# Kernel optimization log

Hardware: AMD Instinct MI355X
Metric: run time of the kernel (lower is better)

## Reference

```python
import jax, jax.numpy as jnp
import numpy as np

B, S, D = 2, 2048, 1024
H = 16
HD = D // H  # head_dim = 64


def setup_inputs() -> dict:
    key = jax.random.key(0)
    ks = jax.random.split(key, 6)
    scale = 0.02
    x = jax.random.normal(ks[0], (B, S, D), dtype=jnp.float32)
    Wq = jax.random.normal(ks[1], (D, D), dtype=jnp.float32) * scale
    Wk = jax.random.normal(ks[2], (D, D), dtype=jnp.float32) * scale
    Wv = jax.random.normal(ks[3], (D, D), dtype=jnp.float32) * scale
    Wo = jax.random.normal(ks[4], (D, D), dtype=jnp.float32) * scale
    bo = jax.random.normal(ks[5], (D,), dtype=jnp.float32) * scale
    return {"x": x, "Wq": Wq, "Wk": Wk, "Wv": Wv, "Wo": Wo, "bo": bo}


def reference(x, Wq, Wk, Wv, Wo, bo):
    b, s, d = x.shape
    # QKV projections (no bias, qkv_bias=False)
    Q = (x @ Wq).reshape(b, s, H, HD)
    K = (x @ Wk).reshape(b, s, H, HD)
    V = (x @ Wv).reshape(b, s, H, HD)
    # [b, h, q, k] attention scores
    scores = jnp.einsum('bqhd,bkhd->bhqk', Q, K)
    # causal mask: positions k > q masked to -inf (applied before scaling, as in source;
    # -inf / sqrt(hd) is still -inf so this matches)
    causal = jnp.triu(jnp.ones((s, s), dtype=bool), k=1)
    scores = jnp.where(causal, -jnp.inf, scores)
    att = jax.nn.softmax(scores / jnp.sqrt(jnp.float32(HD)), axis=-1)
    # dropout p=0.0 -> identity
    ctx = jnp.einsum('bhqk,bkhd->bqhd', att, V).reshape(b, s, d)
    return ctx @ Wo + bo
```

## Files before the change

kernel.cpp:

```cpp
#include <hip/hip_runtime.h>

typedef __bf16 bf16;
typedef __attribute__((ext_vector_type(8))) __bf16 bf16x8;
typedef __attribute__((ext_vector_type(4))) __bf16 bf16x4;
typedef __attribute__((ext_vector_type(4))) float floatx4;

#define MFMA16(a, b, c) __builtin_amdgcn_mfma_f32_16x16x32_bf16((a), (b), (c), 0, 0, 0)

static constexpr int BB = 2, SS = 2048, DD = 1024, HH = 16;
static constexpr int MM = BB * SS;
static constexpr int N_QKV = 3 * DD;

__device__ __forceinline__ float exp2c(float x) {
#if __has_builtin(__builtin_amdgcn_exp2f)
    return __builtin_amdgcn_exp2f(x);
#else
    return exp2f(x);
#endif
}

__device__ __forceinline__ void async16(const void* g, void* l) {
    __builtin_amdgcn_global_load_lds(
        (const __attribute__((address_space(1))) unsigned int*)g,
        (__attribute__((address_space(3))) unsigned int*)l, 16, 0, 0);
}

__global__ __launch_bounds__(256) void prep_kernel(const float* __restrict__ x,
                                                   bf16* __restrict__ xb,
                                                   const float* __restrict__ w0,
                                                   const float* __restrict__ w1,
                                                   const float* __restrict__ w2,
                                                   const float* __restrict__ w3,
                                                   bf16* __restrict__ outT) {
    const int blk = blockIdx.x, tid = threadIdx.x;
    if (blk < 4096) {
        int i = blk * 1024 + tid * 4;
        float4 v = *(const float4*)(x + i);
        bf16x4 o;
        o[0] = (bf16)v.x; o[1] = (bf16)v.y; o[2] = (bf16)v.z; o[3] = (bf16)v.w;
        *(bf16x4*)(xb + i) = o;
    } else {
        __shared__ float tile[32][33];
        const int wblk = blk - 4096;
        const int z = wblk >> 10, rem = wblk & 1023;
        const int by = rem >> 5, bx = rem & 31;
        const int tx = tid & 31, ty = tid >> 5;
        const float* src = (z == 0) ? w0 : (z == 1) ? w1 : (z == 2) ? w2 : w3;
        bf16* dst = outT + (size_t)z * DD * DD;
        int xc = bx * 32 + tx;
        int y0 = by * 32;
        for (int i = ty; i < 32; i += 8)
            tile[i][tx] = src[(size_t)(y0 + i) * DD + xc];
        __syncthreads();
        int xo = y0 + tx;
        int yo0 = bx * 32;
        for (int i = ty; i < 32; i += 8)
            dst[(size_t)(yo0 + i) * DD + xo] = (bf16)tile[tx][i];
    }
}

template <int BM, int BN, bool OUT_BF16, bool FUSE_VT>
__global__ __launch_bounds__(256) void gemm_kernel(const bf16* __restrict__ A,
                                                   const bf16* __restrict__ Bt,
                                                   void* __restrict__ C,
                                                   bf16* __restrict__ Vt_g,
                                                   const float* __restrict__ bias,
                                                   int K, int ldc) {
    constexpr int MT = BM / 32, NT = BN / 32;
    __shared__ bf16 As[BM * 64];
    __shared__ bf16 Bs[BN * 64];
    const int tid = threadIdx.x, wave = tid >> 6, lane = tid & 63;
    const int quad = lane >> 4, l16 = lane & 15;
    const int wm = wave >> 1, wn = wave & 1;
    const int m0 = blockIdx.y * BM, n0 = blockIdx.x * BN;
    const int l8r = lane >> 3, l8c = lane & 7;
    const int gch = ((l8c ^ l8r) * 8);

    floatx4 acc[MT][NT] = {};

    for (int k0 = 0; k0 < K; k0 += 64) {
        __syncthreads();
#pragma unroll
        for (int c = 0; c < BM / 32; ++c) {
            int r = wave * (BM / 4) + c * 8;
            async16(A + (size_t)(m0 + r + l8r) * K + k0 + gch, &As[r * 64]);
        }
#pragma unroll
        for (int c = 0; c < BN / 32; ++c) {
            int r = wave * (BN / 4) + c * 8;
            async16(Bt + (size_t)(n0 + r + l8r) * K + k0 + gch, &Bs[r * 64]);
        }
        __syncthreads();
#pragma unroll
        for (int cc = 0; cc < 2; ++cc) {
            bf16x8 af[MT], bv[NT];
#pragma unroll
            for (int i = 0; i < MT; ++i) {
                int row = wm * (BM / 2) + i * 16 + l16;
                af[i] = *(const bf16x8*)&As[row * 64 + ((cc * 4 + quad) ^ (row & 7)) * 8];
            }
#pragma unroll
            for (int j = 0; j < NT; ++j) {
                int row = wn * (BN / 2) + j * 16 + l16;
                bv[j] = *(const bf16x8*)&Bs[row * 64 + ((cc * 4 + quad) ^ (row & 7)) * 8];
            }
#pragma unroll
            for (int i = 0; i < MT; ++i)
#pragma unroll
                for (int j = 0; j < NT; ++j)
                    acc[i][j] = MFMA16(af[i], bv[j], acc[i][j]);
        }
    }

    if (FUSE_VT && n0 >= 2048) {
#pragma unroll
        for (int i = 0; i < MT; ++i)
#pragma unroll
            for (int j = 0; j < NT; ++j) {
                int grow = m0 + wm * (BM / 2) + i * 16 + quad * 4;
                int gcol = n0 + wn * (BN / 2) + j * 16 + l16;
                int bb = grow >> 11, s = grow & (SS - 1);
                int vcol = gcol - 2048;
                int hh = vcol >> 6, hd = vcol & 63;
                bf16x4 pk;
#pragma unroll
                for (int r = 0; r < 4; ++r) pk[r] = (bf16)acc[i][j][r];
                *(bf16x4*)&Vt_g[(((size_t)(bb * 16 + hh)) * 64 + hd) * SS + s] = pk;
            }
        return;
    }

#pragma unroll
    for (int i = 0; i < MT; ++i)
#pragma unroll
        for (int j = 0; j < NT; ++j)
#pragma unroll
            for (int r = 0; r < 4; ++r) {
                int row = m0 + wm * (BM / 2) + i * 16 + quad * 4 + r;
                int col = n0 + wn * (BN / 2) + j * 16 + l16;
                if (OUT_BF16)
                    ((bf16*)C)[(size_t)row * ldc + col] = (bf16)acc[i][j][r];
                else
                    ((float*)C)[(size_t)row * ldc + col] = acc[i][j][r] + bias[col];
            }
}

__global__ __launch_bounds__(256, 2) void attn_kernel(const bf16* __restrict__ QKV,
                                                      const bf16* __restrict__ Vt_g,
                                                      bf16* __restrict__ ctx) {
    __shared__ __align__(16) bf16 smem[24576];
    bf16* Ks = smem;
    bf16* Vt = smem + 8192;
    bf16* Ps = smem + 16384;
    bf16* Qs = Ps;

    const int tid = threadIdx.x, wave = tid >> 6, lane = tid & 63;
    const int quad = lane >> 4, l16 = lane & 15;
    const int gb = blockIdx.x;
    const int xcd = gb & 7, rr = gb >> 3;
    int bhl, t;
    if (rr < 32) { bhl = rr >> 4;              t = rr & 15; }
    else         { bhl = 2 + ((rr & 31) >> 4); t = 15 - (rr & 15); }
    const int bh = xcd * 4 + bhl;
    const int b = bh >> 4, h = bh & 15;
    const int q0 = t * 128;
    const size_t base = (size_t)(b * SS) * N_QKV;
    const bf16* Vg = Vt_g + (size_t)bh * 64 * SS;
    constexpr float C2 = 0.18033688011112042f;
    const int l8r = lane >> 3, l8c = lane & 7;
    const int gch = (l8c ^ l8r) * 8;
    const int swz = l16 & 7;
    const int nkt = 2 * t + 2;

    {
#pragma unroll
        for (int c = 0; c < 4; ++c) {
            int r0 = wave * 32 + c * 8;
            async16(QKV + base + (size_t)(q0 + r0 + l8r) * N_QKV + h * 64 + gch,
                    Qs + r0 * 64);
        }
#pragma unroll
        for (int c = 0; c < 2; ++c) {
            int r0 = wave * 16 + c * 8;
            async16(QKV + base + (size_t)(r0 + l8r) * N_QKV + DD + h * 64 + gch,
                    Ks + r0 * 64);
            async16(Vg + (size_t)(r0 + l8r) * SS + gch, Vt + r0 * 64);
        }
    }
    __syncthreads();

    bf16x8 qf[2][2];
#pragma unroll
    for (int gg = 0; gg < 2; ++gg)
#pragma unroll
        for (int cc = 0; cc < 2; ++cc) {
            int row = wave * 32 + gg * 16 + l16;
            qf[gg][cc] = *(const bf16x8*)&Qs[row * 64 + ((cc * 4 + quad) ^ swz) * 8];
        }

    bf16x8 onesf = {};
    if (l16 == 0) {
#pragma unroll
        for (int e = 0; e < 8; ++e) onesf[e] = (bf16)1.0f;
    }

    floatx4 accv[2][4] = {};
    floatx4 acc5[2] = {};
    const int qg0 = q0 + wave * 32 + l16;

    for (int kt = 0; kt < nkt; ++kt) {
        const int buf = kt & 1;
        if (kt + 1 < nkt) {
            const int k0n = (kt + 1) * 64;
            const int dst = (buf ^ 1) * 4096;
#pragma unroll
            for (int c = 0; c < 2; ++c) {
                int r0 = wave * 16 + c * 8;
                async16(QKV + base + (size_t)(k0n + r0 + l8r) * N_QKV + DD + h * 64 + gch,
                        Ks + dst + r0 * 64);
                async16(Vg + (size_t)(r0 + l8r) * SS + k0n + gch, Vt + dst + r0 * 64);
            }
        }
        const int k0 = kt * 64;

        floatx4 st[2][4];
#pragma unroll
        for (int j = 0; j < 4; ++j) { st[0][j] = (floatx4){}; st[1][j] = (floatx4){}; }
#pragma unroll
        for (int cc = 0; cc < 2; ++cc)
#pragma unroll
            for (int j = 0; j < 4; ++j) {
                bf16x8 kf = *(const bf16x8*)&Ks[buf * 4096 + (j * 16 + l16) * 64
                                                + ((cc * 4 + quad) ^ swz) * 8];
                st[0][j] = MFMA16(kf, qf[0][cc], st[0][j]);
                st[1][j] = MFMA16(kf, qf[1][cc], st[1][j]);
            }

        if (64 * kt + 63 > q0 + 32 * wave) {
#pragma unroll
            for (int gg = 0; gg < 2; ++gg) {
                const int qq = qg0 + gg * 16;
#pragma unroll
                for (int j = 0; j < 4; ++j) {
                    int kb = k0 + j * 16 + quad * 4;
#pragma unroll
                    for (int r = 0; r < 4; ++r)
                        if (kb + r > qq) st[gg][j][r] = -__builtin_inff();
                }
            }
        }

#pragma unroll
        for (int gg = 0; gg < 2; ++gg)
#pragma unroll
            for (int j = 0; j < 4; ++j) {
                bf16x4 pk4;
#pragma unroll
                for (int r = 0; r < 4; ++r)
                    pk4[r] = (bf16)exp2c(st[gg][j][r] * C2);
                *(bf16x4*)&Ps[wave * 2048 + gg * 1024 + l16 * 64
                              + ((2 * j + (quad >> 1)) ^ swz) * 8 + (quad & 1) * 4] = pk4;
            }

        bf16x8 pf[2][2];
#pragma unroll
        for (int gg = 0; gg < 2; ++gg)
#pragma unroll
            for (int cc = 0; cc < 2; ++cc)
                pf[gg][cc] = *(const bf16x8*)&Ps[wave * 2048 + gg * 1024 + l16 * 64
                                                 + ((cc * 4 + quad) ^ swz) * 8];
#pragma unroll
        for (int cc = 0; cc < 2; ++cc)
#pragma unroll
            for (int j = 0; j < 4; ++j) {
                bf16x8 vt = *(const bf16x8*)&Vt[buf * 4096 + (j * 16 + l16) * 64
                                                + ((cc * 4 + quad) ^ swz) * 8];
                accv[0][j] = MFMA16(pf[0][cc], vt, accv[0][j]);
                accv[1][j] = MFMA16(pf[1][cc], vt, accv[1][j]);
            }
        acc5[0] = MFMA16(pf[0][0], onesf, acc5[0]);
        acc5[0] = MFMA16(pf[0][1], onesf, acc5[0]);
        acc5[1] = MFMA16(pf[1][0], onesf, acc5[1]);
        acc5[1] = MFMA16(pf[1][1], onesf, acc5[1]);

        __syncthreads();
    }

#pragma unroll
    for (int gg = 0; gg < 2; ++gg) {
        float inv[4];
#pragma unroll
        for (int r = 0; r < 4; ++r)
            inv[r] = 1.0f / __shfl(acc5[gg][r], lane & 48, 64);
#pragma unroll
        for (int j = 0; j < 4; ++j)
#pragma unroll
            for (int r = 0; r < 4; ++r) {
                int row = b * SS + q0 + wave * 32 + gg * 16 + quad * 4 + r;
                int col = h * 64 + j * 16 + l16;
                ctx[(size_t)row * DD + col] = (bf16)(accv[gg][j][r] * inv[r]);
            }
    }
}

extern "C" void kernel_launch(void* const* d_in, const int* in_sizes, int n_in,
                              void* d_out, int out_size, void* d_ws, size_t ws_size,
                              hipStream_t stream) {
    const float* x  = (const float*)d_in[0];
    const float* Wq = (const float*)d_in[1];
    const float* Wk = (const float*)d_in[2];
    const float* Wv = (const float*)d_in[3];
    const float* Wo = (const float*)d_in[4];
    const float* bo = (const float*)d_in[5];
    float* out = (float*)d_out;

    char* ws = (char*)d_ws;
    bf16* xb   = (bf16*)ws;
    bf16* WT   = (bf16*)(ws + (size_t)(8  << 20));
    bf16* QKV  = (bf16*)(ws + (size_t)(16 << 20));
    bf16* ctxb = (bf16*)(ws + (size_t)(40 << 20));
    bf16* Vt_g = (bf16*)(ws + (size_t)(48 << 20));

    prep_kernel<<<dim3(8192), dim3(256), 0, stream>>>(x, xb, Wq, Wk, Wv, Wo, WT);
    gemm_kernel<128, 128, true, true><<<dim3(N_QKV / 128, MM / 128), dim3(256), 0, stream>>>(
        xb, WT, QKV, Vt_g, nullptr, DD, N_QKV);
    attn_kernel<<<dim3(512), dim3(256), 0, stream>>>(QKV, Vt_g, ctxb);
    gemm_kernel<128, 64, false, false><<<dim3(DD / 64, MM / 128), dim3(256), 0, stream>>>(
        ctxb, WT + (size_t)3 * DD * DD, out, nullptr, bo, DD, DD);
}
```

Baseline: 173.4 us.

## Shrink attention query tile to 64 rows and double the grid

The attention kernel now handles 64 query rows per block (16 per wave) instead of 128, so it launches 1024 blocks. The per-block LDS footprint shrinks and launch bounds ask for 4 blocks per CU, which should raise occupancy and give finer load balance across the causal triangle. The block-to-tile mapping is reworked with a zigzag pattern across 32 tiles, and masking now runs only on the diagonal tile. In exchange each K/V tile loaded into LDS is reused by half as many query rows, so K/V traffic per unit of work roughly doubles.

```diff
diff --git a/kernel.cpp b/kernel.cpp
--- a/kernel.cpp
+++ b/kernel.cpp
@@ -145,10 +145,10 @@
             }
 }
 
-__global__ __launch_bounds__(256, 2) void attn_kernel(const bf16* __restrict__ QKV,
+__global__ __launch_bounds__(256, 4) void attn_kernel(const bf16* __restrict__ QKV,
                                                       const bf16* __restrict__ Vt_g,
                                                       bf16* __restrict__ ctx) {
-    __shared__ __align__(16) bf16 smem[24576];
+    __shared__ __align__(16) bf16 smem[20480];
     bf16* Ks = smem;
     bf16* Vt = smem + 8192;
     bf16* Ps = smem + 16384;
@@ -158,30 +158,26 @@
     const int quad = lane >> 4, l16 = lane & 15;
     const int gb = blockIdx.x;
     const int xcd = gb & 7, rr = gb >> 3;
-    int bhl, t;
-    if (rr < 32) { bhl = rr >> 4;              t = rr & 15; }
-    else         { bhl = 2 + ((rr & 31) >> 4); t = 15 - (rr & 15); }
-    const int bh = xcd * 4 + bhl;
+    const int hi = rr >> 5, lo = rr & 31;
+    const int t = (hi == 0) ? lo : (hi == 1) ? (31 - lo)
+                : (hi == 2) ? (lo ^ 16) : (31 - (lo ^ 16));
+    const int bh = xcd * 4 + hi;
     const int b = bh >> 4, h = bh & 15;
-    const int q0 = t * 128;
+    const int q0 = t * 64;
     const size_t base = (size_t)(b * SS) * N_QKV;
     const bf16* Vg = Vt_g + (size_t)bh * 64 * SS;
     constexpr float C2 = 0.18033688011112042f;
     const int l8r = lane >> 3, l8c = lane & 7;
     const int gch = (l8c ^ l8r) * 8;
     const int swz = l16 & 7;
-    const int nkt = 2 * t + 2;
+    const int nkt = t + 1;
 
     {
 #pragma unroll
-        for (int c = 0; c < 4; ++c) {
-            int r0 = wave * 32 + c * 8;
+        for (int c = 0; c < 2; ++c) {
+            int r0 = wave * 16 + c * 8;
             async16(QKV + base + (size_t)(q0 + r0 + l8r) * N_QKV + h * 64 + gch,
                     Qs + r0 * 64);
-        }
-#pragma unroll
-        for (int c = 0; c < 2; ++c) {
-            int r0 = wave * 16 + c * 8;
             async16(QKV + base + (size_t)(r0 + l8r) * N_QKV + DD + h * 64 + gch,
                     Ks + r0 * 64);
             async16(Vg + (size_t)(r0 + l8r) * SS + gch, Vt + r0 * 64);
@@ -189,14 +185,12 @@
     }
     __syncthreads();
 
-    bf16x8 qf[2][2];
-#pragma unroll
-    for (int gg = 0; gg < 2; ++gg)
-#pragma unroll
-        for (int cc = 0; cc < 2; ++cc) {
-            int row = wave * 32 + gg * 16 + l16;
-            qf[gg][cc] = *(const bf16x8*)&Qs[row * 64 + ((cc * 4 + quad) ^ swz) * 8];
-        }
+    bf16x8 qf[2];
+#pragma unroll
+    for (int cc = 0; cc < 2; ++cc) {
+        int row = wave * 16 + l16;
+        qf[cc] = *(const bf16x8*)&Qs[row * 64 + ((cc * 4 + quad) ^ swz) * 8];
+    }
 
     bf16x8 onesf = {};
     if (l16 == 0) {
@@ -204,9 +198,9 @@
         for (int e = 0; e < 8; ++e) onesf[e] = (bf16)1.0f;
     }
 
-    floatx4 accv[2][4] = {};
-    floatx4 acc5[2] = {};
-    const int qg0 = q0 + wave * 32 + l16;
+    floatx4 accv[4] = {};
+    floatx4 acc5 = {};
+    const int qg = q0 + wave * 16 + l16;
 
     for (int kt = 0; kt < nkt; ++kt) {
         const int buf = kt & 1;
@@ -223,84 +217,69 @@
         }
         const int k0 = kt * 64;
 
-        floatx4 st[2][4];
-#pragma unroll
-        for (int j = 0; j < 4; ++j) { st[0][j] = (floatx4){}; st[1][j] = (floatx4){}; }
+        floatx4 st[4];
+#pragma unroll
+        for (int j = 0; j < 4; ++j) st[j] = (floatx4){};
 #pragma unroll
         for (int cc = 0; cc < 2; ++cc)
 #pragma unroll
             for (int j = 0; j < 4; ++j) {
                 bf16x8 kf = *(const bf16x8*)&Ks[buf * 4096 + (j * 16 + l16) * 64
                                                 + ((cc * 4 + quad) ^ swz) * 8];
-                st[0][j] = MFMA16(kf, qf[0][cc], st[0][j]);
-                st[1][j] = MFMA16(kf, qf[1][cc], st[1][j]);
-            }
-
-        if (64 * kt + 63 > q0 + 32 * wave) {
-#pragma unroll
-            for (int gg = 0; gg < 2; ++gg) {
-                const int qq = qg0 + gg * 16;
-#pragma unroll
-                for (int j = 0; j < 4; ++j) {
-                    int kb = k0 + j * 16 + quad * 4;
-#pragma unroll
-                    for (int r = 0; r < 4; ++r)
-                        if (kb + r > qq) st[gg][j][r] = -__builtin_inff();
-                }
-            }
-        }
-
-#pragma unroll
-        for (int gg = 0; gg < 2; ++gg)
+                st[j] = MFMA16(kf, qf[cc], st[j]);
+            }
+
+        if (kt == nkt - 1) {
 #pragma unroll
             for (int j = 0; j < 4; ++j) {
-                bf16x4 pk4;
+                int kb = k0 + j * 16 + quad * 4;
 #pragma unroll
                 for (int r = 0; r < 4; ++r)
-                    pk4[r] = (bf16)exp2c(st[gg][j][r] * C2);
-                *(bf16x4*)&Ps[wave * 2048 + gg * 1024 + l16 * 64
-                              + ((2 * j + (quad >> 1)) ^ swz) * 8 + (quad & 1) * 4] = pk4;
-            }
-
-        bf16x8 pf[2][2];
-#pragma unroll
-        for (int gg = 0; gg < 2; ++gg)
-#pragma unroll
-            for (int cc = 0; cc < 2; ++cc)
-                pf[gg][cc] = *(const bf16x8*)&Ps[wave * 2048 + gg * 1024 + l16 * 64
-                                                 + ((cc * 4 + quad) ^ swz) * 8];
+                    if (kb + r > qg) st[j][r] = -__builtin_inff();
+            }
+        }
+
+#pragma unroll
+        for (int j = 0; j < 4; ++j) {
+            bf16x4 pk4;
+#pragma unroll
+            for (int r = 0; r < 4; ++r)
+                pk4[r] = (bf16)exp2c(st[j][r] * C2);
+            *(bf16x4*)&Ps[wave * 1024 + l16 * 64
+                          + ((2 * j + (quad >> 1)) ^ swz) * 8 + (quad & 1) * 4] = pk4;
+        }
+
+        bf16x8 pf[2];
+#pragma unroll
+        for (int cc = 0; cc < 2; ++cc)
+            pf[cc] = *(const bf16x8*)&Ps[wave * 1024 + l16 * 64
+                                         + ((cc * 4 + quad) ^ swz) * 8];
 #pragma unroll
         for (int cc = 0; cc < 2; ++cc)
 #pragma unroll
             for (int j = 0; j < 4; ++j) {
                 bf16x8 vt = *(const bf16x8*)&Vt[buf * 4096 + (j * 16 + l16) * 64
                                                 + ((cc * 4 + quad) ^ swz) * 8];
-                accv[0][j] = MFMA16(pf[0][cc], vt, accv[0][j]);
-                accv[1][j] = MFMA16(pf[1][cc], vt, accv[1][j]);
-            }
-        acc5[0] = MFMA16(pf[0][0], onesf, acc5[0]);
-        acc5[0] = MFMA16(pf[0][1], onesf, acc5[0]);
-        acc5[1] = MFMA16(pf[1][0], onesf, acc5[1]);
-        acc5[1] = MFMA16(pf[1][1], onesf, acc5[1]);
+                accv[j] = MFMA16(pf[cc], vt, accv[j]);
+            }
+        acc5 = MFMA16(pf[0], onesf, acc5);
+        acc5 = MFMA16(pf[1], onesf, acc5);
 
         __syncthreads();
     }
 
-#pragma unroll
-    for (int gg = 0; gg < 2; ++gg) {
-        float inv[4];
-#pragma unroll
-        for (int r = 0; r < 4; ++r)
-            inv[r] = 1.0f / __shfl(acc5[gg][r], lane & 48, 64);
-#pragma unroll
-        for (int j = 0; j < 4; ++j)
-#pragma unroll
-            for (int r = 0; r < 4; ++r) {
-                int row = b * SS + q0 + wave * 32 + gg * 16 + quad * 4 + r;
-                int col = h * 64 + j * 16 + l16;
-                ctx[(size_t)row * DD + col] = (bf16)(accv[gg][j][r] * inv[r]);
-            }
-    }
+    float inv[4];
+#pragma unroll
+    for (int r = 0; r < 4; ++r)
+        inv[r] = 1.0f / __shfl(acc5[r], lane & 48, 64);
+#pragma unroll
+    for (int j = 0; j < 4; ++j)
+#pragma unroll
+        for (int r = 0; r < 4; ++r) {
+            int row = b * SS + q0 + wave * 16 + quad * 4 + r;
+            int col = h * 64 + j * 16 + l16;
+            ctx[(size_t)row * DD + col] = (bf16)(accv[j][r] * inv[r]);
+        }
 }
 
 extern "C" void kernel_launch(void* const* d_in, const int* in_sizes, int n_in,
@@ -324,7 +303,7 @@
     prep_kernel<<<dim3(8192), dim3(256), 0, stream>>>(x, xb, Wq, Wk, Wv, Wo, WT);
     gemm_kernel<128, 128, true, true><<<dim3(N_QKV / 128, MM / 128), dim3(256), 0, stream>>>(
         xb, WT, QKV, Vt_g, nullptr, DD, N_QKV);
-    attn_kernel<<<dim3(512), dim3(256), 0, stream>>>(QKV, Vt_g, ctxb);
+    attn_kernel<<<dim3(1024), dim3(256), 0, stream>>>(QKV, Vt_g, ctxb);
     gemm_kernel<128, 64, false, false><<<dim3(DD / 64, MM / 128), dim3(256), 0, stream>>>(
         ctxb, WT + (size_t)3 * DD * DD, out, nullptr, bo, DD, DD);
 }
```

Result: no change. 170.9 us, median of 2 (-1.5%).
